# Optimization experiments

Measured on AMD Instinct MI355X. Metric: run time of the kernel, lower is better.

The kernel has to match this reference:

```python
import jax, jax.numpy as jnp
import numpy as np

N = 50000       # nodes
E = 1600000     # edges (avg degree 32)
IN = 64         # in_channels
ED = 16         # edge_dim
H = 128         # hidden_channels


def setup_inputs() -> dict:
    key = jax.random.key(0)
    ks = jax.random.split(key, 32)
    rn = lambda k, shape, s: jax.random.normal(k, shape, jnp.float32) * s
    inp = {}
    inp['x'] = rn(ks[0], (N, IN), 1.0)
    inp['edge_index'] = jax.random.randint(ks[1], (2, E), 0, N, dtype=jnp.int64)
    inp['edge_attr'] = rn(ks[2], (E, ED), 1.0)
    # per-layer params: edge linear (ED -> node_dim), MLP (d_in->H, H->H)
    node_dims = [IN, H, H]
    i = 3
    for l, d in enumerate(node_dims):
        inp[f'We{l}'] = rn(ks[i], (ED, d), 1.0 / np.sqrt(ED)); i += 1
        inp[f'be{l}'] = jnp.zeros((d,), jnp.float32)
        inp[f'W1_{l}'] = rn(ks[i], (d, H), 1.0 / np.sqrt(d)); i += 1
        inp[f'b1_{l}'] = jnp.zeros((H,), jnp.float32)
        inp[f'W2_{l}'] = rn(ks[i], (H, H), 1.0 / np.sqrt(H)); i += 1
        inp[f'b2_{l}'] = jnp.zeros((H,), jnp.float32)
    inp['Wlin'] = rn(ks[i], (H, 1), 1.0 / np.sqrt(H))
    inp['blin'] = jnp.zeros((1,), jnp.float32)
    return inp


def gine_conv(x, src, dst, ea, We, be, W1, b1, W2, b2):
    # message: relu(x_j + Lin_e(edge_attr)); aggregate: sum into dst; eps=0
    msg = jax.nn.relu(x[src] + ea @ We + be)            # [E, d]
    agg = jax.ops.segment_sum(msg, dst, num_segments=x.shape[0])  # [N, d]
    h = x + agg                                          # (1+eps)*x + agg, eps=0
    return jax.nn.relu(h @ W1 + b1) @ W2 + b2            # MLP


def reference(x, edge_index, edge_attr,
              We0, be0, W1_0, b1_0, W2_0, b2_0,
              We1, be1, W1_1, b1_1, W2_1, b2_1,
              We2, be2, W1_2, b1_2, W2_2, b2_2,
              Wlin, blin):
    src, dst = edge_index[0], edge_index[1]
    h = jax.nn.relu(gine_conv(x, src, dst, edge_attr, We0, be0, W1_0, b1_0, W2_0, b2_0))
    h = jax.nn.relu(gine_conv(h, src, dst, edge_attr, We1, be1, W1_1, b1_1, W2_1, b2_1))
    h = jax.nn.relu(gine_conv(h, src, dst, edge_attr, We2, be2, W1_2, b1_2, W2_2, b2_2))
    out = jax.nn.sigmoid(h @ Wlin + blin)                # [N, 1]
    return out.squeeze(-1)                               # [N]
```

## Files before the change

kernel.cpp:

```cpp
#include <hip/hip_runtime.h>
#include <math.h>


#define BLK 256

typedef __attribute__((ext_vector_type(2))) float f32x2;

__device__ inline f32x2 pk_fma(f32x2 a, f32x2 b, f32x2 c) {
    f32x2 d;
    asm("v_pk_fma_f32 %0, %1, %2, %3" : "=v"(d) : "v"(a), "v"(b), "v"(c));
    return d;
}


__global__ void detect_kernel(const unsigned int* __restrict__ ei, int* __restrict__ flag) {
    int t = blockIdx.x * blockDim.x + threadIdx.x;
    if (t < 1024) {
        if (ei[2 * t + 1] != 0u) atomicOr(flag, 1);
    }
}

__global__ void convert_hist_kernel(const int* __restrict__ ei32, const long long* __restrict__ ei64,
                                    const int* __restrict__ flag, int E,
                                    int* __restrict__ src, unsigned int* __restrict__ drank,
                                    int* __restrict__ counts) {
    int e = blockIdx.x * blockDim.x + threadIdx.x;
    if (e >= E) return;
    int s, d;
    if (*flag) { s = ei32[e]; d = ei32[E + e]; }
    else       { s = (int)ei64[e]; d = (int)ei64[E + e]; }
    src[e] = s;
    unsigned int r = (unsigned int)atomicAdd(&counts[d], 1);
    drank[e] = (unsigned int)d | (r << 16);
}

__global__ void scan_kernel(const int* __restrict__ counts, int* __restrict__ offsets, int n) {
    __shared__ int tsum[256];
    __shared__ int texcl[256];
    int t = threadIdx.x;
    int chunk = (n + 255) >> 8;
    int b = t * chunk, e = min(b + chunk, n);
    int s = 0;
    for (int i = b; i < e; i++) s += counts[i];
    tsum[t] = s;
    __syncthreads();
    if (t == 0) {
        int run = 0;
        for (int i = 0; i < 256; i++) { texcl[i] = run; run += tsum[i]; }
        offsets[n] = run;
    }
    __syncthreads();
    int run = texcl[t];
    for (int i = b; i < e; i++) { offsets[i] = run; run += counts[i]; }
}

__global__ void scatter_perm_kernel(const unsigned int* __restrict__ drank,
                                    const int* __restrict__ offsets,
                                    int* __restrict__ perm, int E) {
    int e = blockIdx.x * blockDim.x + threadIdx.x;
    if (e >= E) return;
    unsigned int v = drank[e];
    perm[offsets[v & 0xffffu] + (int)(v >> 16)] = e;
}

__global__ __launch_bounds__(256) void gather_ea_kernel(
    const int* __restrict__ perm, const int* __restrict__ src32,
    const float4* __restrict__ ea4,
    int* __restrict__ srcp, float4* __restrict__ eap4, int E) {
    int t = blockIdx.x * blockDim.x + threadIdx.x;
    int p = t >> 2, q = t & 3;
    if (p >= E) return;
    int e = perm[p];
    if (q == 0) srcp[p] = src32[e];
    eap4[(size_t)p * 4 + q] = ea4[(size_t)e * 4 + q];
}

template <int D>
__global__ __launch_bounds__(256) void aggregate_kernel(
    const float* __restrict__ x, const float* __restrict__ eap,
    const int* __restrict__ srcp,
    const float* __restrict__ We, const float* __restrict__ be,
    const int* __restrict__ offsets,
    float* __restrict__ h, int n) {
    constexpr int C = D / 64;
    int lane = threadIdx.x & 63;
    int node = __builtin_amdgcn_readfirstlane(blockIdx.x * 4 + (threadIdx.x >> 6));
    if (node >= n) return;
    int c0 = lane * C;

    f32x2 wp[C][8];
#pragma unroll
    for (int j = 0; j < C; j++)
#pragma unroll
        for (int t = 0; t < 8; t++) {
            f32x2 v; v.x = We[(2 * t) * D + c0 + j]; v.y = We[(2 * t + 1) * D + c0 + j];
            wp[j][t] = v;
        }
    float bias[C], acc[C];
#pragma unroll
    for (int j = 0; j < C; j++) {
        bias[j] = be[c0 + j];
        acc[j] = x[(size_t)node * D + c0 + j];
    }
    int p = offsets[node], pe = offsets[node + 1];

    for (; p + 4 <= pe; p += 4) {
        int s0 = srcp[p], s1 = srcp[p + 1], s2 = srcp[p + 2], s3 = srcp[p + 3];
        float xv[4][C];
        {
            const float* r0 = x + (size_t)s0 * D + c0;
            const float* r1 = x + (size_t)s1 * D + c0;
            const float* r2 = x + (size_t)s2 * D + c0;
            const float* r3 = x + (size_t)s3 * D + c0;
            if constexpr (C == 2) {
                float2 t0 = *(const float2*)r0, t1 = *(const float2*)r1;
                float2 t2 = *(const float2*)r2, t3 = *(const float2*)r3;
                xv[0][0] = t0.x; xv[0][1] = t0.y; xv[1][0] = t1.x; xv[1][1] = t1.y;
                xv[2][0] = t2.x; xv[2][1] = t2.y; xv[3][0] = t3.x; xv[3][1] = t3.y;
            } else {
                xv[0][0] = *r0; xv[1][0] = *r1; xv[2][0] = *r2; xv[3][0] = *r3;
            }
        }
#pragma unroll
        for (int u = 0; u < 4; u++) {
            const float4* er = (const float4*)(eap + (size_t)(p + u) * 16);
            float4 e0 = er[0], e1 = er[1], e2 = er[2], e3 = er[3];
            f32x2 ev[8];
            ev[0].x = e0.x; ev[0].y = e0.y;  ev[1].x = e0.z; ev[1].y = e0.w;
            ev[2].x = e1.x; ev[2].y = e1.y;  ev[3].x = e1.z; ev[3].y = e1.w;
            ev[4].x = e2.x; ev[4].y = e2.y;  ev[5].x = e2.z; ev[5].y = e2.w;
            ev[6].x = e3.x; ev[6].y = e3.y;  ev[7].x = e3.z; ev[7].y = e3.w;
#pragma unroll
            for (int j = 0; j < C; j++) {
                f32x2 prod; prod.x = xv[u][j] + bias[j]; prod.y = 0.f;
#pragma unroll
                for (int t = 0; t < 8; t++) prod = pk_fma(ev[t], wp[j][t], prod);
                acc[j] += fmaxf(prod.x + prod.y, 0.f);
            }
        }
    }
    for (; p < pe; p++) {
        int s = srcp[p];
        const float* xr = x + (size_t)s * D + c0;
        float xv[C];
        if constexpr (C == 2) { float2 t = *(const float2*)xr; xv[0] = t.x; xv[1] = t.y; }
        else xv[0] = *xr;
        const float4* er = (const float4*)(eap + (size_t)p * 16);
        float4 e0 = er[0], e1 = er[1], e2 = er[2], e3 = er[3];
        f32x2 ev[8];
        ev[0].x = e0.x; ev[0].y = e0.y;  ev[1].x = e0.z; ev[1].y = e0.w;
        ev[2].x = e1.x; ev[2].y = e1.y;  ev[3].x = e1.z; ev[3].y = e1.w;
        ev[4].x = e2.x; ev[4].y = e2.y;  ev[5].x = e2.z; ev[5].y = e2.w;
        ev[6].x = e3.x; ev[6].y = e3.y;  ev[7].x = e3.z; ev[7].y = e3.w;
#pragma unroll
        for (int j = 0; j < C; j++) {
            f32x2 prod; prod.x = xv[j] + bias[j]; prod.y = 0.f;
#pragma unroll
            for (int t = 0; t < 8; t++) prod = pk_fma(ev[t], wp[j][t], prod);
            acc[j] += fmaxf(prod.x + prod.y, 0.f);
        }
    }
#pragma unroll
    for (int j = 0; j < C; j++) h[(size_t)node * D + c0 + j] = acc[j];
}

template <int K>
__global__ __launch_bounds__(256) void gemm_kernel(
    const float* __restrict__ A, const float* __restrict__ B,
    const float* __restrict__ bias, float* __restrict__ C, int n) {
    __shared__ __align__(16) float As[16][68];
    __shared__ __align__(16) float Bs[16][128];
    int t = threadIdx.x;
    int row0 = blockIdx.x * 64;
    int tr = t >> 5, tc = t & 31;
    float acc[8][4];
#pragma unroll
    for (int r = 0; r < 8; r++)
#pragma unroll
        for (int c = 0; c < 4; c++) acc[r][c] = 0.f;

    int lr = t >> 2, lk = (t & 3) * 4;
    int bk = t >> 4, bc = (t & 15) * 8;

    int grow = row0 + lr;
    const float* aptr = A + (size_t)grow * K + lk;
    float4 a;
    if (grow < n) a = *(const float4*)aptr;
    else a = make_float4(0.f, 0.f, 0.f, 0.f);
    const float4* bp = (const float4*)(B + (size_t)bk * 128 + bc);
    float4 b0 = bp[0], b1 = bp[1];

#pragma unroll 1
    for (int ks = 0; ks < K; ks += 16) {
        As[lk + 0][lr] = a.x; As[lk + 1][lr] = a.y;
        As[lk + 2][lr] = a.z; As[lk + 3][lr] = a.w;
        *(float4*)&Bs[bk][bc] = b0;
        *(float4*)&Bs[bk][bc + 4] = b1;
        __syncthreads();
        if (ks + 16 < K) {
            if (grow < n) a = *(const float4*)(aptr + ks + 16);
            const float4* bp2 = (const float4*)(B + (size_t)(ks + 16 + bk) * 128 + bc);
            b0 = bp2[0]; b1 = bp2[1];
        }
#pragma unroll
        for (int kk = 0; kk < 16; kk++) {
            float4 a0 = *(const float4*)&As[kk][tr * 8];
            float4 a1 = *(const float4*)&As[kk][tr * 8 + 4];
            float4 bv = *(const float4*)&Bs[kk][tc * 4];
            float ar[8] = {a0.x, a0.y, a0.z, a0.w, a1.x, a1.y, a1.z, a1.w};
            float bc4[4] = {bv.x, bv.y, bv.z, bv.w};
#pragma unroll
            for (int r = 0; r < 8; r++)
#pragma unroll
                for (int c = 0; c < 4; c++) acc[r][c] = fmaf(ar[r], bc4[c], acc[r][c]);
        }
        __syncthreads();
    }
    float4 bb = *(const float4*)(bias + tc * 4);
#pragma unroll
    for (int r = 0; r < 8; r++) {
        int gr = row0 + tr * 8 + r;
        if (gr < n) {
            float4 v;
            v.x = fmaxf(acc[r][0] + bb.x, 0.f);
            v.y = fmaxf(acc[r][1] + bb.y, 0.f);
            v.z = fmaxf(acc[r][2] + bb.z, 0.f);
            v.w = fmaxf(acc[r][3] + bb.w, 0.f);
            *(float4*)(C + (size_t)gr * 128 + tc * 4) = v;
        }
    }
}

__global__ __launch_bounds__(256) void final_kernel(
    const float* __restrict__ x, const float* __restrict__ Wlin,
    const float* __restrict__ blin, float* __restrict__ out, int n) {
    int lane = threadIdx.x & 63;
    int node = blockIdx.x * 4 + (threadIdx.x >> 6);
    if (node >= n) return;
    float2 w = *(const float2*)(Wlin + lane * 2);
    float2 xv = *(const float2*)(x + (size_t)node * 128 + lane * 2);
    float v = xv.x * w.x + xv.y * w.y;
#pragma unroll
    for (int off = 32; off; off >>= 1) v += __shfl_down(v, off, 64);
    if (lane == 0) out[node] = 1.f / (1.f + expf(-(v + blin[0])));
}

extern "C" void kernel_launch(void* const* d_in, const int* in_sizes, int n_in,
                              void* d_out, int out_size, void* d_ws, size_t ws_size,
                              hipStream_t stream) {
    const float* x_in = (const float*)d_in[0];
    const void* ei    = d_in[1];
    const float* ea   = (const float*)d_in[2];
    const float* We[3]  = {(const float*)d_in[3], (const float*)d_in[9],  (const float*)d_in[15]};
    const float* be[3]  = {(const float*)d_in[4], (const float*)d_in[10], (const float*)d_in[16]};
    const float* W1[3]  = {(const float*)d_in[5], (const float*)d_in[11], (const float*)d_in[17]};
    const float* b1[3]  = {(const float*)d_in[6], (const float*)d_in[12], (const float*)d_in[18]};
    const float* W2[3]  = {(const float*)d_in[7], (const float*)d_in[13], (const float*)d_in[19]};
    const float* b2[3]  = {(const float*)d_in[8], (const float*)d_in[14], (const float*)d_in[20]};
    const float* Wlin = (const float*)d_in[21];
    const float* blin = (const float*)d_in[22];
    float* out = (float*)d_out;

    const int N = in_sizes[0] / 64;
    const int E = in_sizes[1] / 2;

    size_t off = 0;
    auto alloc = [&](size_t bytes) {
        void* p = (char*)d_ws + off;
        off += (bytes + 255) & ~(size_t)255;
        return p;
    };
    int*          flag    = (int*)alloc(4);
    int*          src32   = (int*)alloc((size_t)E * 4);
    unsigned int* drank   = (unsigned int*)alloc((size_t)E * 4);
    int*          counts  = (int*)alloc((size_t)N * 4);
    int*          offsets = (int*)alloc((size_t)(N + 1) * 4);
    int*          perm    = (int*)alloc((size_t)E * 4);
    int*          srcp    = (int*)alloc((size_t)E * 4);
    float*        eap     = (float*)alloc((size_t)E * 16 * 4);
    float*        bufA    = (float*)alloc((size_t)N * 128 * 4);
    float*        bufB    = (float*)alloc((size_t)N * 128 * 4);
    float*        bufC    = (float*)alloc((size_t)N * 128 * 4);

    hipMemsetAsync(flag, 0, 4, stream);
    hipMemsetAsync(counts, 0, (size_t)N * 4, stream);

    int egrid = (E + BLK - 1) / BLK;
    detect_kernel<<<4, BLK, 0, stream>>>((const unsigned int*)ei, flag);
    convert_hist_kernel<<<egrid, BLK, 0, stream>>>((const int*)ei, (const long long*)ei, flag, E,
                                                   src32, drank, counts);
    scan_kernel<<<1, BLK, 0, stream>>>(counts, offsets, N);
    scatter_perm_kernel<<<egrid, BLK, 0, stream>>>(drank, offsets, perm, E);
    int g4grid = ((E * 4) + BLK - 1) / BLK;
    gather_ea_kernel<<<g4grid, BLK, 0, stream>>>(perm, src32, (const float4*)ea,
                                                 srcp, (float4*)eap, E);

    int ngrid4 = (N + 3) / 4;
    int ggrid  = (N + 63) / 64;

    aggregate_kernel<64><<<ngrid4, BLK, 0, stream>>>(x_in, eap, srcp, We[0], be[0], offsets, bufA, N);
    gemm_kernel<64><<<ggrid, BLK, 0, stream>>>(bufA, W1[0], b1[0], bufB, N);
    gemm_kernel<128><<<ggrid, BLK, 0, stream>>>(bufB, W2[0], b2[0], bufC, N);
    aggregate_kernel<128><<<ngrid4, BLK, 0, stream>>>(bufC, eap, srcp, We[1], be[1], offsets, bufA, N);
    gemm_kernel<128><<<ggrid, BLK, 0, stream>>>(bufA, W1[1], b1[1], bufB, N);
    gemm_kernel<128><<<ggrid, BLK, 0, stream>>>(bufB, W2[1], b2[1], bufC, N);
    aggregate_kernel<128><<<ngrid4, BLK, 0, stream>>>(bufC, eap, srcp, We[2], be[2], offsets, bufA, N);
    gemm_kernel<128><<<ggrid, BLK, 0, stream>>>(bufA, W1[2], b1[2], bufB, N);
    gemm_kernel<128><<<ggrid, BLK, 0, stream>>>(bufB, W2[2], b2[2], bufC, N);

    final_kernel<<<ngrid4, BLK, 0, stream>>>(bufC, Wlin, blin, out, N);
}
```

Measured before the change: 943.4 us.

## Shrink GEMM row tile to 32 and read src indices directly in gather

Halves the GEMM block row tile from 64 to 32 rows, with 4x4 accumulators per thread, so the grid has twice as many blocks and each thread holds fewer registers. This spreads work over more CUs, at the cost of less reuse of the B tile per block. Separately, the histogram kernel no longer writes an intermediate src32 array; the gather kernel reads source indices straight from edge_index in its int32 or int64 form. That saves one E-sized write and read, but makes the src read a random gather.

```diff
diff --git a/kernel.cpp b/kernel.cpp
--- a/kernel.cpp
+++ b/kernel.cpp
@@ -22,14 +22,13 @@
 
 __global__ void convert_hist_kernel(const int* __restrict__ ei32, const long long* __restrict__ ei64,
                                     const int* __restrict__ flag, int E,
-                                    int* __restrict__ src, unsigned int* __restrict__ drank,
+                                    unsigned int* __restrict__ drank,
                                     int* __restrict__ counts) {
     int e = blockIdx.x * blockDim.x + threadIdx.x;
     if (e >= E) return;
-    int s, d;
-    if (*flag) { s = ei32[e]; d = ei32[E + e]; }
-    else       { s = (int)ei64[e]; d = (int)ei64[E + e]; }
-    src[e] = s;
+    int d;
+    if (*flag) d = ei32[E + e];
+    else       d = (int)ei64[E + e];
     unsigned int r = (unsigned int)atomicAdd(&counts[d], 1);
     drank[e] = (unsigned int)d | (r << 16);
 }
@@ -64,14 +63,21 @@
 }
 
 __global__ __launch_bounds__(256) void gather_ea_kernel(
-    const int* __restrict__ perm, const int* __restrict__ src32,
+    const int* __restrict__ perm,
+    const int* __restrict__ ei32, const long long* __restrict__ ei64,
+    const int* __restrict__ flag,
     const float4* __restrict__ ea4,
     int* __restrict__ srcp, float4* __restrict__ eap4, int E) {
     int t = blockIdx.x * blockDim.x + threadIdx.x;
     int p = t >> 2, q = t & 3;
     if (p >= E) return;
     int e = perm[p];
-    if (q == 0) srcp[p] = src32[e];
+    if (q == 0) {
+        int s;
+        if (*flag) s = ei32[e];
+        else       s = (int)ei64[e];
+        srcp[p] = s;
+    }
     eap4[(size_t)p * 4 + q] = ea4[(size_t)e * 4 + q];
 }
 
@@ -168,49 +174,47 @@
 __global__ __launch_bounds__(256) void gemm_kernel(
     const float* __restrict__ A, const float* __restrict__ B,
     const float* __restrict__ bias, float* __restrict__ C, int n) {
-    __shared__ __align__(16) float As[16][68];
+    __shared__ __align__(16) float As[16][36];
     __shared__ __align__(16) float Bs[16][128];
     int t = threadIdx.x;
-    int row0 = blockIdx.x * 64;
+    int row0 = blockIdx.x * 32;
     int tr = t >> 5, tc = t & 31;
-    float acc[8][4];
-#pragma unroll
-    for (int r = 0; r < 8; r++)
+    float acc[4][4];
+#pragma unroll
+    for (int r = 0; r < 4; r++)
 #pragma unroll
         for (int c = 0; c < 4; c++) acc[r][c] = 0.f;
 
-    int lr = t >> 2, lk = (t & 3) * 4;
+    int lr = t & 31, lk = (t >> 5) * 2;
     int bk = t >> 4, bc = (t & 15) * 8;
 
     int grow = row0 + lr;
     const float* aptr = A + (size_t)grow * K + lk;
-    float4 a;
-    if (grow < n) a = *(const float4*)aptr;
-    else a = make_float4(0.f, 0.f, 0.f, 0.f);
+    float2 a;
+    if (grow < n) a = *(const float2*)aptr;
+    else a = make_float2(0.f, 0.f);
     const float4* bp = (const float4*)(B + (size_t)bk * 128 + bc);
     float4 b0 = bp[0], b1 = bp[1];
 
 #pragma unroll 1
     for (int ks = 0; ks < K; ks += 16) {
         As[lk + 0][lr] = a.x; As[lk + 1][lr] = a.y;
-        As[lk + 2][lr] = a.z; As[lk + 3][lr] = a.w;
         *(float4*)&Bs[bk][bc] = b0;
         *(float4*)&Bs[bk][bc + 4] = b1;
         __syncthreads();
         if (ks + 16 < K) {
-            if (grow < n) a = *(const float4*)(aptr + ks + 16);
+            if (grow < n) a = *(const float2*)(aptr + ks + 16);
             const float4* bp2 = (const float4*)(B + (size_t)(ks + 16 + bk) * 128 + bc);
             b0 = bp2[0]; b1 = bp2[1];
         }
 #pragma unroll
         for (int kk = 0; kk < 16; kk++) {
-            float4 a0 = *(const float4*)&As[kk][tr * 8];
-            float4 a1 = *(const float4*)&As[kk][tr * 8 + 4];
+            float4 a0 = *(const float4*)&As[kk][tr * 4];
             float4 bv = *(const float4*)&Bs[kk][tc * 4];
-            float ar[8] = {a0.x, a0.y, a0.z, a0.w, a1.x, a1.y, a1.z, a1.w};
+            float ar[4] = {a0.x, a0.y, a0.z, a0.w};
             float bc4[4] = {bv.x, bv.y, bv.z, bv.w};
 #pragma unroll
-            for (int r = 0; r < 8; r++)
+            for (int r = 0; r < 4; r++)
 #pragma unroll
                 for (int c = 0; c < 4; c++) acc[r][c] = fmaf(ar[r], bc4[c], acc[r][c]);
         }
@@ -218,8 +222,8 @@
     }
     float4 bb = *(const float4*)(bias + tc * 4);
 #pragma unroll
-    for (int r = 0; r < 8; r++) {
-        int gr = row0 + tr * 8 + r;
+    for (int r = 0; r < 4; r++) {
+        int gr = row0 + tr * 4 + r;
         if (gr < n) {
             float4 v;
             v.x = fmaxf(acc[r][0] + bb.x, 0.f);
@@ -271,7 +275,6 @@
         return p;
     };
     int*          flag    = (int*)alloc(4);
-    int*          src32   = (int*)alloc((size_t)E * 4);
     unsigned int* drank   = (unsigned int*)alloc((size_t)E * 4);
     int*          counts  = (int*)alloc((size_t)N * 4);
     int*          offsets = (int*)alloc((size_t)(N + 1) * 4);
@@ -288,15 +291,15 @@
     int egrid = (E + BLK - 1) / BLK;
     detect_kernel<<<4, BLK, 0, stream>>>((const unsigned int*)ei, flag);
     convert_hist_kernel<<<egrid, BLK, 0, stream>>>((const int*)ei, (const long long*)ei, flag, E,
-                                                   src32, drank, counts);
+                                                   drank, counts);
     scan_kernel<<<1, BLK, 0, stream>>>(counts, offsets, N);
     scatter_perm_kernel<<<egrid, BLK, 0, stream>>>(drank, offsets, perm, E);
     int g4grid = ((E * 4) + BLK - 1) / BLK;
-    gather_ea_kernel<<<g4grid, BLK, 0, stream>>>(perm, src32, (const float4*)ea,
-                                                 srcp, (float4*)eap, E);
+    gather_ea_kernel<<<g4grid, BLK, 0, stream>>>(perm, (const int*)ei, (const long long*)ei, flag,
+                                                 (const float4*)ea, srcp, (float4*)eap, E);
 
     int ngrid4 = (N + 3) / 4;
-    int ggrid  = (N + 63) / 64;
+    int ggrid  = (N + 31) / 32;
 
     aggregate_kernel<64><<<ngrid4, BLK, 0, stream>>>(x_in, eap, srcp, We[0], be[0], offsets, bufA, N);
     gemm_kernel<64><<<ggrid, BLK, 0, stream>>>(bufA, W1[0], b1[0], bufB, N);
```

After: 939.5 us. No clear change (-0.4%).
